# Kernel optimization log

Hardware: AMD Instinct MI355X
Metric: run time of the kernel (lower is better)

## Reference

```python
import jax, jax.numpy as jnp
import numpy as np

N_NODES = 50_000
N_EDGES = 1_600_000
IN_HIDDEN = 256
OUT_HIDDEN = 32
EDGE_HIDDEN = 64
NHEAD = 4
N_EDGE_TYPES = 8
NEG_SLOPE = 0.2


def _glorot(key, shape):
    stdv = np.sqrt(6.0 / (shape[-2] + shape[-1]))
    return jax.random.uniform(key, shape, jnp.float32, -stdv, stdv)


def setup_inputs() -> dict:
    key = jax.random.key(0)
    ks = jax.random.split(key, 10)
    src = jax.random.randint(ks[0], (N_EDGES,), 0, N_NODES, dtype=jnp.int32)
    trg = jax.random.randint(ks[1], (N_EDGES,), 0, N_NODES, dtype=jnp.int32)
    etype = jax.random.randint(ks[2], (N_EDGES,), 0, N_EDGE_TYPES, dtype=jnp.int32)
    edge = jnp.stack([src, trg, etype], axis=0)  # [3, E]
    x = jax.random.normal(ks[3], (N_NODES, IN_HIDDEN), jnp.float32)
    return {
        "edge": edge,
        "x": x,
        "edge_emb": _glorot(ks[4], (N_EDGE_TYPES, EDGE_HIDDEN)),
        "W": _glorot(ks[5], (IN_HIDDEN, OUT_HIDDEN * NHEAD)),
        "W_e": _glorot(ks[6], (EDGE_HIDDEN, EDGE_HIDDEN * NHEAD)),
        "a_l": _glorot(ks[7], (1, NHEAD, OUT_HIDDEN)),
        "a_r": _glorot(ks[8], (1, NHEAD, OUT_HIDDEN)),
        "a_e": _glorot(ks[9], (1, NHEAD, EDGE_HIDDEN)),
    }


def reference(edge, x, edge_emb, W, W_e, a_l, a_r, a_e):
    num_nodes = x.shape[0]
    src, trg, etype = edge[0], edge[1], edge[2]

    # node / edge-type projections
    h = (x @ W).reshape(num_nodes, NHEAD, OUT_HIDDEN)          # [N, H, D]
    h = jnp.where(jnp.isnan(h), 0.0, h)
    e = (edge_emb @ W_e).reshape(N_EDGE_TYPES, NHEAD, EDGE_HIDDEN)  # [T, H, De]

    # per-node / per-type attention logits, gathered to edges -> [E, H]
    h_l = (a_l * h).sum(-1)[src]
    h_r = (a_r * h).sum(-1)[trg]
    h_e = (a_e * e).sum(-1)[etype]
    scores = jax.nn.leaky_relu(h_l + h_r + h_e, NEG_SLOPE)     # [E, H]

    # neighborhood-aware softmax (global max shift, as in original)
    exp_scores = jnp.exp(scores - jnp.max(scores))
    denom = jax.ops.segment_sum(exp_scores, trg, num_segments=num_nodes)  # [N, H]
    attn = (exp_scores / (denom[trg] + 1e-16))[:, :, None]     # [E, H, 1]

    # weighted aggregation: scatter-add messages to targets
    msgs = h[src] * attn                                       # [E, H, D]
    out = jax.ops.segment_sum(msgs, trg, num_segments=num_nodes)  # [N, H, D]
    return out, attn
```

## Files before the change

### kernel.cpp

```cpp
#include <hip/hip_runtime.h>
#include <hip/hip_bf16.h>
#include <hip/hip_fp16.h>

#define N_NODES 50000
#define N_EDGES 1600000
#define IN_H 256
#define NHEAD 4
#define EDGE_H 64
#define N_ET 8


typedef __attribute__((ext_vector_type(8))) short bf16x8v;
typedef __attribute__((ext_vector_type(4))) float f32x4;

__device__ __forceinline__ float ldT(const float* p) { return *p; }
__device__ __forceinline__ float ldT(const __hip_bfloat16* p) { return __bfloat162float(*p); }
__device__ __forceinline__ void stT(float* p, float v) { *p = v; }
__device__ __forceinline__ void stT(__hip_bfloat16* p, float v) { *p = __float2bfloat16(v); }

__device__ __forceinline__ short f2bs(float f) {
    __hip_bfloat16 b = __float2bfloat16(f);
    return (short)__builtin_bit_cast(unsigned short, b);
}
__device__ __forceinline__ float bs2f(short s) {
    return __uint_as_float(((unsigned)(unsigned short)s) << 16);
}

__device__ __forceinline__ unsigned enc_f32(float f) {
    unsigned u = __float_as_uint(f);
    return (u & 0x80000000u) ? ~u : (u | 0x80000000u);
}
__device__ __forceinline__ float dec_f32(unsigned u) {
    return __uint_as_float((u & 0x80000000u) ? (u & 0x7fffffffu) : ~u);
}
__device__ __forceinline__ float lrelu(float v) { return v > 0.f ? v : 0.2f * v; }

__device__ __forceinline__ unsigned pack_h2(float a, float b) {
    unsigned lo = (unsigned)__half_as_ushort(__float2half(a));
    unsigned hi = (unsigned)__half_as_ushort(__float2half(b));
    return lo | (hi << 16);
}
__device__ __forceinline__ float2 unpack_h2(int w) {
    __half2 h = __builtin_bit_cast(__half2, w);
    return __half22float2(h);
}

__global__ void k_detect(const unsigned* __restrict__ xw, int* __restrict__ flag) {
    int lane = threadIdx.x;
    int cnt = 0;
    for (int i = lane; i < 1024; i += 64) {
        unsigned e = (xw[i] >> 23) & 255u;
        if (e >= 64u && e <= 160u) cnt++;
    }
    for (int off = 32; off; off >>= 1) cnt += __shfl_xor(cnt, off);
    if (lane == 0) *flag = (cnt > 512) ? 1 : 0;
}

template<typename T, int EXPECT>
__global__ __launch_bounds__(256) void k_setup(
        const void* __restrict__ Wv, const void* __restrict__ embv,
        const void* __restrict__ Wev, const void* __restrict__ aev,
        __hip_bfloat16* __restrict__ Wt, float* __restrict__ h_e,
        unsigned* __restrict__ hemax, const int* __restrict__ flag) {
    if (*flag != EXPECT) return;
    const T* W   = (const T*)Wv;
    const T* emb = (const T*)embv;
    const T* We  = (const T*)Wev;
    const T* ae  = (const T*)aev;
    if (blockIdx.x == 0) {
        for (int i = threadIdx.x; i < 128 * 256; i += 256) {
            int c = i >> 8, k = i & 255;
            Wt[i] = __float2bfloat16(ldT(W + k * 128 + c));
        }
        return;
    }
    int ty = blockIdx.x - 1;
    int t = threadIdx.x, lane = t & 63;
    float acc = 0.f;
    for (int k = 0; k < EDGE_H; ++k)
        acc += ldT(emb + ty * EDGE_H + k) * ldT(We + k * 256 + t);
    float v = ldT(ae + t) * acc;
    for (int off = 32; off; off >>= 1) v += __shfl_xor(v, off);
    if (lane == 0) {
        h_e[ty * NHEAD + (t >> 6)] = v;
        atomicMax(&hemax[t >> 6], enc_f32(v));
    }
}

template<typename T, int EXPECT>
__global__ __launch_bounds__(256) void k_proj(const void* __restrict__ xv,
        const __hip_bfloat16* __restrict__ Wt, __hip_bfloat16* __restrict__ h,
        float* __restrict__ hl, float* __restrict__ hr,
        const void* __restrict__ alv, const void* __restrict__ arv,
        const int* __restrict__ edge, int* __restrict__ counts8,
        const int* __restrict__ flag) {
    if (*flag != EXPECT) return;
    {
        int q = blockIdx.x & 7;
        int base = blockIdx.x * 1024;
        int lim = min(base + 1024, N_EDGES);
        int* cnt = counts8 + q * 50000;
        for (int i = base + threadIdx.x; i < lim; i += 256)
            atomicAdd(&cnt[edge[N_EDGES + i]], 1);
    }
    const T* x  = (const T*)xv;
    const T* al = (const T*)alv;
    const T* ar = (const T*)arv;
    int wid = threadIdx.x >> 6, lane = threadIdx.x & 63;
    int rg = blockIdx.x * 2 + (wid >> 1);
    if (rg >= 3125) return;
    int toff = (wid & 1) * 4;
    int r0 = rg * 16;
    int r = lane & 15;
    int kb = (lane >> 4) * 8;
    const T* xrow = x + (size_t)(r0 + r) * IN_H;
    f32x4 z = {0.f, 0.f, 0.f, 0.f};
    f32x4 acc[4];
#pragma unroll
    for (int t = 0; t < 4; ++t) acc[t] = z;
#pragma unroll
    for (int kk = 0; kk < 8; ++kk) {
        int k0 = kk * 32 + kb;
        bf16x8v a;
        if constexpr (sizeof(T) == 4) {
            float4 lo = *(const float4*)(xrow + k0);
            float4 hi = *(const float4*)(xrow + k0 + 4);
            a[0] = f2bs(lo.x); a[1] = f2bs(lo.y); a[2] = f2bs(lo.z); a[3] = f2bs(lo.w);
            a[4] = f2bs(hi.x); a[5] = f2bs(hi.y); a[6] = f2bs(hi.z); a[7] = f2bs(hi.w);
        } else {
            a = *(const bf16x8v*)(xrow + k0);
        }
#pragma unroll
        for (int t = 0; t < 4; ++t) {
            bf16x8v b = *(const bf16x8v*)(Wt + ((toff + t) * 16 + r) * 256 + k0);
            acc[t] = __builtin_amdgcn_mfma_f32_16x16x32_bf16(a, b, acc[t], 0, 0, 0);
        }
    }
    float alc[4], arc[4];
#pragma unroll
    for (int t = 0; t < 4; ++t) {
        alc[t] = ldT(al + (toff + t) * 16 + r);
        arc[t] = ldT(ar + (toff + t) * 16 + r);
    }
    int ob = (lane >> 4) * 4;
    float pl[2][4] = {{0,0,0,0},{0,0,0,0}}, pr[2][4] = {{0,0,0,0},{0,0,0,0}};
#pragma unroll
    for (int t = 0; t < 4; ++t) {
        int col = (toff + t) * 16 + r;
#pragma unroll
        for (int g = 0; g < 4; ++g) {
            float v = acc[t][g];
            if (v != v) v = 0.f;
            h[(size_t)(r0 + ob + g) * 128 + col] = __float2bfloat16(v);
            pl[t >> 1][g] += alc[t] * v;
            pr[t >> 1][g] += arc[t] * v;
        }
    }
#pragma unroll
    for (int hh = 0; hh < 2; ++hh)
#pragma unroll
        for (int g = 0; g < 4; ++g) {
            float vl = pl[hh][g], vr = pr[hh][g];
#pragma unroll
            for (int off = 8; off; off >>= 1) {
                vl += __shfl_xor(vl, off);
                vr += __shfl_xor(vr, off);
            }
            if (r == 0) {
                int node = r0 + ob + g;
                hl[node * 4 + (toff >> 1) + hh] = vl;
                hr[node * 4 + (toff >> 1) + hh] = vr;
            }
        }
}

__global__ __launch_bounds__(256) void k_maxred(
        const float* __restrict__ hl, unsigned* __restrict__ hlmax) {
    const float NEG = -3.4e38f;
    float4 ml = {NEG, NEG, NEG, NEG};
    for (int n = blockIdx.x * 256 + threadIdx.x; n < N_NODES; n += 128 * 256) {
        float4 a = *(const float4*)(hl + n * 4);
        ml.x = fmaxf(ml.x, a.x); ml.y = fmaxf(ml.y, a.y);
        ml.z = fmaxf(ml.z, a.z); ml.w = fmaxf(ml.w, a.w);
    }
#pragma unroll
    for (int off = 32; off; off >>= 1) {
        ml.x = fmaxf(ml.x, __shfl_xor(ml.x, off));
        ml.y = fmaxf(ml.y, __shfl_xor(ml.y, off));
        ml.z = fmaxf(ml.z, __shfl_xor(ml.z, off));
        ml.w = fmaxf(ml.w, __shfl_xor(ml.w, off));
    }
    if ((threadIdx.x & 63) == 0) {
        atomicMax(&hlmax[0], enc_f32(ml.x)); atomicMax(&hlmax[1], enc_f32(ml.y));
        atomicMax(&hlmax[2], enc_f32(ml.z)); atomicMax(&hlmax[3], enc_f32(ml.w));
    }
}


__global__ __launch_bounds__(256) void k_scanA(
        const int* __restrict__ counts8, int* __restrict__ node_tot,
        int* __restrict__ blk_sum) {
    int n = blockIdx.x * 256 + threadIdx.x;
    int tot = 0;
    if (n < N_NODES) {
#pragma unroll
        for (int q = 0; q < 8; ++q) tot += counts8[q * 50000 + n];
        node_tot[n] = tot;
    }
    __shared__ int red[256];
    red[threadIdx.x] = tot;
    __syncthreads();
    for (int off = 128; off; off >>= 1) {
        if (threadIdx.x < off) red[threadIdx.x] += red[threadIdx.x + off];
        __syncthreads();
    }
    if (threadIdx.x == 0) blk_sum[blockIdx.x] = red[0];
}

__global__ __launch_bounds__(256) void k_scanB(
        const int* __restrict__ blk_sum, int* __restrict__ blk_base,
        int* __restrict__ offsets) {
    __shared__ int ps[256];
    int t = threadIdx.x;
    int v = (t < 196) ? blk_sum[t] : 0;
    ps[t] = v;
    __syncthreads();
    for (int off = 1; off < 256; off <<= 1) {
        int u = (t >= off) ? ps[t - off] : 0;
        __syncthreads();
        ps[t] += u;
        __syncthreads();
    }
    if (t < 196) blk_base[t] = ps[t] - v;
    if (t == 255) offsets[N_NODES] = ps[255];
}

__global__ __launch_bounds__(256) void k_scanC(
        const int* __restrict__ counts8, const int* __restrict__ node_tot,
        const int* __restrict__ blk_base, int* __restrict__ offsets,
        int* __restrict__ off8) {
    __shared__ int ps[256];
    int t = threadIdx.x;
    int n = blockIdx.x * 256 + t;
    int v = (n < N_NODES) ? node_tot[n] : 0;
    ps[t] = v;
    __syncthreads();
    for (int off = 1; off < 256; off <<= 1) {
        int u = (t >= off) ? ps[t - off] : 0;
        __syncthreads();
        ps[t] += u;
        __syncthreads();
    }
    if (n < N_NODES) {
        int base = blk_base[blockIdx.x] + ps[t] - v;
        offsets[n] = base;
#pragma unroll
        for (int q = 0; q < 8; ++q) {
            off8[q * 50000 + n] = base;
            base += counts8[q * 50000 + n];
        }
    }
}

__global__ __launch_bounds__(256) void k_build(
        const int* __restrict__ edge, const int* __restrict__ off8,
        int* __restrict__ cursor8,
        const float* __restrict__ hl, const float* __restrict__ hr,
        const float* __restrict__ he,
        const unsigned* __restrict__ hlmax, const unsigned* __restrict__ hemax,
        int* __restrict__ rec) {
    float G0 = dec_f32(hlmax[0]) + dec_f32(hemax[0]);
    float G1 = dec_f32(hlmax[1]) + dec_f32(hemax[1]);
    float G2 = dec_f32(hlmax[2]) + dec_f32(hemax[2]);
    float G3 = dec_f32(hlmax[3]) + dec_f32(hemax[3]);
    int q = blockIdx.x & 7;
    const int* offq = off8 + q * 50000;
    int* curq = cursor8 + q * 50000;
    int base = blockIdx.x * 1024;
    int lim = min(base + 1024, N_EDGES);
    for (int e = base + threadIdx.x; e < lim; e += 256) {
        int s = edge[e], t = edge[N_EDGES + e], ty = edge[2 * N_EDGES + e];
        int pos = offq[t] + atomicAdd(&curq[t], 1);
        float4 a = *(const float4*)(hl + s * 4);
        float4 b = *(const float4*)(hr + t * 4);
        float4 c = *(const float4*)(he + ty * 4);
        float p0 = __expf(lrelu(a.x + b.x + c.x) - lrelu(G0 + b.x));
        float p1 = __expf(lrelu(a.y + b.y + c.y) - lrelu(G1 + b.y));
        float p2 = __expf(lrelu(a.z + b.z + c.z) - lrelu(G2 + b.z));
        float p3 = __expf(lrelu(a.w + b.w + c.w) - lrelu(G3 + b.w));
        int4 w;
        w.x = (int)pack_h2(p0, p1);
        w.y = (int)pack_h2(p2, p3);
        w.z = s;
        w.w = e;
        *(int4*)(rec + (size_t)pos * 4) = w;
    }
}

template<typename OUTT, int EXPECT>
__global__ __launch_bounds__(256) void k_agg(
        const int* __restrict__ rec, const int* __restrict__ offsets,
        const __hip_bfloat16* __restrict__ h, void* __restrict__ outv,
        const int* __restrict__ flag) {
    if (*flag != EXPECT) return;
    OUTT* out = (OUTT*)outv;
    int node = (blockIdx.x << 2) + (threadIdx.x >> 6);
    if (node >= N_NODES) return;
    int lane = threadIdx.x & 63;
    int beg = offsets[node], end = offsets[node + 1];

    float d0 = 0.f, d1 = 0.f, d2 = 0.f, d3 = 0.f;
    for (int j = beg + lane; j < end; j += 64) {
        int2 w = *(const int2*)(rec + (size_t)j * 4);
        float2 f01 = unpack_h2(w.x);
        float2 f23 = unpack_h2(w.y);
        d0 += f01.x; d1 += f01.y; d2 += f23.x; d3 += f23.y;
    }
#pragma unroll
    for (int off = 32; off; off >>= 1) {
        d0 += __shfl_xor(d0, off); d1 += __shfl_xor(d1, off);
        d2 += __shfl_xor(d2, off); d3 += __shfl_xor(d3, off);
    }
    float inv0 = 1.f / (d0 + 1e-16f), inv1 = 1.f / (d1 + 1e-16f);
    float inv2 = 1.f / (d2 + 1e-16f), inv3 = 1.f / (d3 + 1e-16f);

    int sub = lane >> 4;
    int l16 = lane & 15;
    int hd  = l16 >> 2;
    float invd = hd == 0 ? inv0 : hd == 1 ? inv1 : hd == 2 ? inv2 : inv3;
    float inva = l16 == 0 ? inv0 : l16 == 1 ? inv1 : l16 == 2 ? inv2 : inv3;
    OUTT* attn_out = out + (size_t)N_NODES * 128;

    float acc[8] = {0.f, 0.f, 0.f, 0.f, 0.f, 0.f, 0.f, 0.f};
    for (int jg = beg; jg < end; jg += 4) {
        int j = jg + sub;
        bool valid = j < end;
        int jc = valid ? j : end - 1;
        int4 w = *(const int4*)(rec + (size_t)jc * 4);
        float2 f01 = unpack_h2(w.x);
        float2 f23 = unpack_h2(w.y);
        int s = w.z;
        if (valid && l16 < 4) {
            float ph = l16 == 0 ? f01.x : l16 == 1 ? f01.y : l16 == 2 ? f23.x : f23.y;
            stT(&attn_out[(size_t)w.w * 4 + l16], ph * inva);
        }
        float phd = hd == 0 ? f01.x : hd == 1 ? f01.y : hd == 2 ? f23.x : f23.y;
        float wgt = valid ? phd * invd : 0.f;
        bf16x8v hv = *(const bf16x8v*)(h + (size_t)s * 128 + l16 * 8);
#pragma unroll
        for (int i = 0; i < 8; ++i) acc[i] += bs2f(hv[i]) * wgt;
    }
#pragma unroll
    for (int i = 0; i < 8; ++i) {
        acc[i] += __shfl_xor(acc[i], 16);
        acc[i] += __shfl_xor(acc[i], 32);
    }
    if (sub == 0) {
#pragma unroll
        for (int i = 0; i < 8; ++i)
            stT(&out[(size_t)node * 128 + l16 * 8 + i], acc[i]);
    }
}

extern "C" void kernel_launch(void* const* d_in, const int* in_sizes, int n_in,
                              void* d_out, int out_size, void* d_ws, size_t ws_size,
                              hipStream_t stream) {
    const int* edge = (const int*)d_in[0];
    const void* x   = d_in[1];
    const void* emb = d_in[2];
    const void* W   = d_in[3];
    const void* We  = d_in[4];
    const void* al  = d_in[5];
    const void* ar  = d_in[6];
    const void* ae  = d_in[7];

    float* ws = (float*)d_ws;
    int* counts8    = (int*)ws;
    int* cursor8    = counts8 + 400000;
    unsigned* hlmax = (unsigned*)(counts8 + 800000);
    unsigned* hemax = (unsigned*)(counts8 + 800008);
    int* flag       = counts8 + 800012;
    float* hl       = ws + 800064;
    float* hr       = ws + 1000064;
    int* offsets    = (int*)ws + 1200064;
    int* off8       = (int*)ws + 1250112;
    int* node_tot   = (int*)ws + 1650112;
    int* blk_sum    = (int*)ws + 1700112;
    int* blk_base   = (int*)ws + 1700368;
    float* he       = ws + 1700624;
    __hip_bfloat16* Wt = (__hip_bfloat16*)(ws + 1700656);
    int* rec        = (int*)ws + 1717040;
    __hip_bfloat16* h = (__hip_bfloat16*)(ws + 8117040);

    hipMemsetAsync(ws, 0, (size_t)800064 * 4, stream);

    k_detect<<<1, 64, 0, stream>>>((const unsigned*)x, flag);

    k_setup<float, 1><<<1 + N_ET, 256, 0, stream>>>(W, emb, We, ae, Wt, he,
                                                    hemax, flag);
    k_setup<__hip_bfloat16, 0><<<1 + N_ET, 256, 0, stream>>>(W, emb, We, ae, Wt,
                                                             he, hemax, flag);

    k_proj<float, 1><<<1563, 256, 0, stream>>>(x, Wt, h, hl, hr, al, ar,
                                               edge, counts8, flag);
    k_proj<__hip_bfloat16, 0><<<1563, 256, 0, stream>>>(x, Wt, h, hl, hr,
                                                        al, ar, edge, counts8, flag);

    k_maxred<<<128, 256, 0, stream>>>(hl, hlmax);
    k_scanA<<<196, 256, 0, stream>>>(counts8, node_tot, blk_sum);
    k_scanB<<<1, 256, 0, stream>>>(blk_sum, blk_base, offsets);
    k_scanC<<<196, 256, 0, stream>>>(counts8, node_tot, blk_base, offsets, off8);
    k_build<<<1563, 256, 0, stream>>>(edge, off8, cursor8, hl, hr, he,
                                      hlmax, hemax, rec);

    k_agg<float, 1><<<12500, 256, 0, stream>>>(rec, offsets, h, d_out, flag);
    k_agg<__hip_bfloat16, 0><<<12500, 256, 0, stream>>>(rec, offsets, h,
                                                        d_out, flag);
}
```

Measured before the change: 453.3 us.

## Compute softmax denominators via atomics in build and write attention in edge order

Folds the max reduction into the scan kernel. The build kernel now accumulates per-target denominators with float atomics into 8 partitioned buffers, plus a per-edge copy of the probabilities, and a new reduction kernel sums the partitions. Attention output is written by a separate edge-ordered kernel with coalesced stores, which replaces scattered writes from the aggregation kernel. The aggregation no longer makes a denominator pass. The cost is 4 float atomics per edge, extra p_by_e traffic, a larger memset, and two more launches.

```diff
diff --git a/kernel.cpp b/kernel.cpp
--- a/kernel.cpp
+++ b/kernel.cpp
@@ -174,38 +174,20 @@
         }
 }
 
-__global__ __launch_bounds__(256) void k_maxred(
-        const float* __restrict__ hl, unsigned* __restrict__ hlmax) {
+
+__global__ __launch_bounds__(256) void k_scanA(
+        const int* __restrict__ counts8, int* __restrict__ node_tot,
+        int* __restrict__ blk_sum, const float* __restrict__ hl,
+        unsigned* __restrict__ hlmax) {
+    int n = blockIdx.x * 256 + threadIdx.x;
+    int tot = 0;
     const float NEG = -3.4e38f;
     float4 ml = {NEG, NEG, NEG, NEG};
-    for (int n = blockIdx.x * 256 + threadIdx.x; n < N_NODES; n += 128 * 256) {
-        float4 a = *(const float4*)(hl + n * 4);
-        ml.x = fmaxf(ml.x, a.x); ml.y = fmaxf(ml.y, a.y);
-        ml.z = fmaxf(ml.z, a.z); ml.w = fmaxf(ml.w, a.w);
-    }
-#pragma unroll
-    for (int off = 32; off; off >>= 1) {
-        ml.x = fmaxf(ml.x, __shfl_xor(ml.x, off));
-        ml.y = fmaxf(ml.y, __shfl_xor(ml.y, off));
-        ml.z = fmaxf(ml.z, __shfl_xor(ml.z, off));
-        ml.w = fmaxf(ml.w, __shfl_xor(ml.w, off));
-    }
-    if ((threadIdx.x & 63) == 0) {
-        atomicMax(&hlmax[0], enc_f32(ml.x)); atomicMax(&hlmax[1], enc_f32(ml.y));
-        atomicMax(&hlmax[2], enc_f32(ml.z)); atomicMax(&hlmax[3], enc_f32(ml.w));
-    }
-}
-
-
-__global__ __launch_bounds__(256) void k_scanA(
-        const int* __restrict__ counts8, int* __restrict__ node_tot,
-        int* __restrict__ blk_sum) {
-    int n = blockIdx.x * 256 + threadIdx.x;
-    int tot = 0;
     if (n < N_NODES) {
 #pragma unroll
         for (int q = 0; q < 8; ++q) tot += counts8[q * 50000 + n];
         node_tot[n] = tot;
+        ml = *(const float4*)(hl + n * 4);
     }
     __shared__ int red[256];
     red[threadIdx.x] = tot;
@@ -215,6 +197,17 @@
         __syncthreads();
     }
     if (threadIdx.x == 0) blk_sum[blockIdx.x] = red[0];
+#pragma unroll
+    for (int off = 32; off; off >>= 1) {
+        ml.x = fmaxf(ml.x, __shfl_xor(ml.x, off));
+        ml.y = fmaxf(ml.y, __shfl_xor(ml.y, off));
+        ml.z = fmaxf(ml.z, __shfl_xor(ml.z, off));
+        ml.w = fmaxf(ml.w, __shfl_xor(ml.w, off));
+    }
+    if ((threadIdx.x & 63) == 0) {
+        atomicMax(&hlmax[0], enc_f32(ml.x)); atomicMax(&hlmax[1], enc_f32(ml.y));
+        atomicMax(&hlmax[2], enc_f32(ml.z)); atomicMax(&hlmax[3], enc_f32(ml.w));
+    }
 }
 
 __global__ __launch_bounds__(256) void k_scanB(
@@ -264,11 +257,11 @@
 
 __global__ __launch_bounds__(256) void k_build(
         const int* __restrict__ edge, const int* __restrict__ off8,
-        int* __restrict__ cursor8,
+        int* __restrict__ cursor8, float* __restrict__ denom8,
         const float* __restrict__ hl, const float* __restrict__ hr,
         const float* __restrict__ he,
         const unsigned* __restrict__ hlmax, const unsigned* __restrict__ hemax,
-        int* __restrict__ rec) {
+        int* __restrict__ rec, int* __restrict__ p_by_e) {
     float G0 = dec_f32(hlmax[0]) + dec_f32(hemax[0]);
     float G1 = dec_f32(hlmax[1]) + dec_f32(hemax[1]);
     float G2 = dec_f32(hlmax[2]) + dec_f32(hemax[2]);
@@ -276,6 +269,7 @@
     int q = blockIdx.x & 7;
     const int* offq = off8 + q * 50000;
     int* curq = cursor8 + q * 50000;
+    float* denq = denom8 + q * 200000;
     int base = blockIdx.x * 1024;
     int lim = min(base + 1024, N_EDGES);
     for (int e = base + threadIdx.x; e < lim; e += 256) {
@@ -292,16 +286,53 @@
         w.x = (int)pack_h2(p0, p1);
         w.y = (int)pack_h2(p2, p3);
         w.z = s;
-        w.w = e;
+        w.w = 0;
         *(int4*)(rec + (size_t)pos * 4) = w;
-    }
+        *(int2*)(p_by_e + (size_t)e * 2) = make_int2(w.x, w.y);
+        atomicAdd(&denq[t * 4 + 0], p0);
+        atomicAdd(&denq[t * 4 + 1], p1);
+        atomicAdd(&denq[t * 4 + 2], p2);
+        atomicAdd(&denq[t * 4 + 3], p3);
+    }
+}
+
+__global__ __launch_bounds__(256) void k_sumden(
+        const float* __restrict__ denom8, float* __restrict__ denom) {
+    int n = blockIdx.x * 256 + threadIdx.x;
+    if (n >= N_NODES) return;
+    float4 d = {0.f, 0.f, 0.f, 0.f};
+#pragma unroll
+    for (int q = 0; q < 8; ++q) {
+        float4 v = *(const float4*)(denom8 + q * 200000 + n * 4);
+        d.x += v.x; d.y += v.y; d.z += v.z; d.w += v.w;
+    }
+    *(float4*)(denom + n * 4) = d;
+}
+
+template<typename OUTT, int EXPECT>
+__global__ __launch_bounds__(256) void k_attn(
+        const int* __restrict__ p_by_e, const int* __restrict__ edge,
+        const float* __restrict__ denom, void* __restrict__ outv,
+        const int* __restrict__ flag) {
+    if (*flag != EXPECT) return;
+    int e = blockIdx.x * 256 + threadIdx.x;
+    int t = edge[N_EDGES + e];
+    float4 d = *(const float4*)(denom + t * 4);
+    int2 w = *(const int2*)(p_by_e + (size_t)e * 2);
+    float2 f01 = unpack_h2(w.x);
+    float2 f23 = unpack_h2(w.y);
+    OUTT* attn_out = (OUTT*)outv + (size_t)N_NODES * 128;
+    stT(&attn_out[(size_t)e * 4 + 0], f01.x / (d.x + 1e-16f));
+    stT(&attn_out[(size_t)e * 4 + 1], f01.y / (d.y + 1e-16f));
+    stT(&attn_out[(size_t)e * 4 + 2], f23.x / (d.z + 1e-16f));
+    stT(&attn_out[(size_t)e * 4 + 3], f23.y / (d.w + 1e-16f));
 }
 
 template<typename OUTT, int EXPECT>
 __global__ __launch_bounds__(256) void k_agg(
         const int* __restrict__ rec, const int* __restrict__ offsets,
-        const __hip_bfloat16* __restrict__ h, void* __restrict__ outv,
-        const int* __restrict__ flag) {
+        const float* __restrict__ denom, const __hip_bfloat16* __restrict__ h,
+        void* __restrict__ outv, const int* __restrict__ flag) {
     if (*flag != EXPECT) return;
     OUTT* out = (OUTT*)outv;
     int node = (blockIdx.x << 2) + (threadIdx.x >> 6);
@@ -309,42 +340,25 @@
     int lane = threadIdx.x & 63;
     int beg = offsets[node], end = offsets[node + 1];
 
-    float d0 = 0.f, d1 = 0.f, d2 = 0.f, d3 = 0.f;
-    for (int j = beg + lane; j < end; j += 64) {
-        int2 w = *(const int2*)(rec + (size_t)j * 4);
-        float2 f01 = unpack_h2(w.x);
-        float2 f23 = unpack_h2(w.y);
-        d0 += f01.x; d1 += f01.y; d2 += f23.x; d3 += f23.y;
-    }
-#pragma unroll
-    for (int off = 32; off; off >>= 1) {
-        d0 += __shfl_xor(d0, off); d1 += __shfl_xor(d1, off);
-        d2 += __shfl_xor(d2, off); d3 += __shfl_xor(d3, off);
-    }
-    float inv0 = 1.f / (d0 + 1e-16f), inv1 = 1.f / (d1 + 1e-16f);
-    float inv2 = 1.f / (d2 + 1e-16f), inv3 = 1.f / (d3 + 1e-16f);
+    float4 dn = *(const float4*)(denom + node * 4);
+    float inv0 = 1.f / (dn.x + 1e-16f), inv1 = 1.f / (dn.y + 1e-16f);
+    float inv2 = 1.f / (dn.z + 1e-16f), inv3 = 1.f / (dn.w + 1e-16f);
 
     int sub = lane >> 4;
     int l16 = lane & 15;
     int hd  = l16 >> 2;
     float invd = hd == 0 ? inv0 : hd == 1 ? inv1 : hd == 2 ? inv2 : inv3;
-    float inva = l16 == 0 ? inv0 : l16 == 1 ? inv1 : l16 == 2 ? inv2 : inv3;
-    OUTT* attn_out = out + (size_t)N_NODES * 128;
 
     float acc[8] = {0.f, 0.f, 0.f, 0.f, 0.f, 0.f, 0.f, 0.f};
     for (int jg = beg; jg < end; jg += 4) {
         int j = jg + sub;
         bool valid = j < end;
         int jc = valid ? j : end - 1;
-        int4 w = *(const int4*)(rec + (size_t)jc * 4);
-        float2 f01 = unpack_h2(w.x);
-        float2 f23 = unpack_h2(w.y);
-        int s = w.z;
-        if (valid && l16 < 4) {
-            float ph = l16 == 0 ? f01.x : l16 == 1 ? f01.y : l16 == 2 ? f23.x : f23.y;
-            stT(&attn_out[(size_t)w.w * 4 + l16], ph * inva);
-        }
-        float phd = hd == 0 ? f01.x : hd == 1 ? f01.y : hd == 2 ? f23.x : f23.y;
+        const int* rp = rec + (size_t)jc * 4;
+        int pw = (hd < 2) ? rp[0] : rp[1];
+        int s = rp[2];
+        float2 f = unpack_h2(pw);
+        float phd = (hd & 1) ? f.y : f.x;
         float wgt = valid ? phd * invd : 0.f;
         bf16x8v hv = *(const bf16x8v*)(h + (size_t)s * 128 + l16 * 8);
 #pragma unroll
@@ -377,22 +391,25 @@
     float* ws = (float*)d_ws;
     int* counts8    = (int*)ws;
     int* cursor8    = counts8 + 400000;
-    unsigned* hlmax = (unsigned*)(counts8 + 800000);
-    unsigned* hemax = (unsigned*)(counts8 + 800008);
-    int* flag       = counts8 + 800012;
-    float* hl       = ws + 800064;
-    float* hr       = ws + 1000064;
-    int* offsets    = (int*)ws + 1200064;
-    int* off8       = (int*)ws + 1250112;
-    int* node_tot   = (int*)ws + 1650112;
-    int* blk_sum    = (int*)ws + 1700112;
-    int* blk_base   = (int*)ws + 1700368;
-    float* he       = ws + 1700624;
-    __hip_bfloat16* Wt = (__hip_bfloat16*)(ws + 1700656);
-    int* rec        = (int*)ws + 1717040;
-    __hip_bfloat16* h = (__hip_bfloat16*)(ws + 8117040);
-
-    hipMemsetAsync(ws, 0, (size_t)800064 * 4, stream);
+    float* denom8   = ws + 800000;
+    unsigned* hlmax = (unsigned*)(ws + 2400000);
+    unsigned* hemax = (unsigned*)(ws + 2400008);
+    int* flag       = (int*)ws + 2400012;
+    float* hl       = ws + 2400064;
+    float* hr       = ws + 2600064;
+    int* offsets    = (int*)ws + 2800064;
+    int* off8       = (int*)ws + 2850112;
+    int* node_tot   = (int*)ws + 3250112;
+    int* blk_sum    = (int*)ws + 3300112;
+    int* blk_base   = (int*)ws + 3300368;
+    float* he       = ws + 3300624;
+    __hip_bfloat16* Wt = (__hip_bfloat16*)(ws + 3300656);
+    int* p_by_e     = (int*)ws + 3317040;
+    float* denom    = ws + 6517040;
+    int* rec        = (int*)ws + 6717040;
+    __hip_bfloat16* h = (__hip_bfloat16*)(ws + 13117040);
+
+    hipMemsetAsync(ws, 0, (size_t)2400064 * 4, stream);
 
     k_detect<<<1, 64, 0, stream>>>((const unsigned*)x, flag);
 
@@ -406,14 +423,18 @@
     k_proj<__hip_bfloat16, 0><<<1563, 256, 0, stream>>>(x, Wt, h, hl, hr,
                                                         al, ar, edge, counts8, flag);
 
-    k_maxred<<<128, 256, 0, stream>>>(hl, hlmax);
-    k_scanA<<<196, 256, 0, stream>>>(counts8, node_tot, blk_sum);
+    k_scanA<<<196, 256, 0, stream>>>(counts8, node_tot, blk_sum, hl, hlmax);
     k_scanB<<<1, 256, 0, stream>>>(blk_sum, blk_base, offsets);
     k_scanC<<<196, 256, 0, stream>>>(counts8, node_tot, blk_base, offsets, off8);
-    k_build<<<1563, 256, 0, stream>>>(edge, off8, cursor8, hl, hr, he,
-                                      hlmax, hemax, rec);
-
-    k_agg<float, 1><<<12500, 256, 0, stream>>>(rec, offsets, h, d_out, flag);
-    k_agg<__hip_bfloat16, 0><<<12500, 256, 0, stream>>>(rec, offsets, h,
+    k_build<<<1563, 256, 0, stream>>>(edge, off8, cursor8, denom8, hl, hr, he,
+                                      hlmax, hemax, rec, p_by_e);
+    k_sumden<<<196, 256, 0, stream>>>(denom8, denom);
+
+    k_attn<float, 1><<<6250, 256, 0, stream>>>(p_by_e, edge, denom, d_out, flag);
+    k_attn<__hip_bfloat16, 0><<<6250, 256, 0, stream>>>(p_by_e, edge, denom,
                                                         d_out, flag);
-}
+
+    k_agg<float, 1><<<12500, 256, 0, stream>>>(rec, offsets, denom, h, d_out, flag);
+    k_agg<__hip_bfloat16, 0><<<12500, 256, 0, stream>>>(rec, offsets, denom, h,
+                                                        d_out, flag);
+}
```

New measurement: 740.3 us. +63.3%, slower.
